# Kernel optimization log

Measured on AMD Instinct MI355X. Metric: run time of the kernel, lower is better.

The kernel has to match this reference:

```python
import jax, jax.numpy as jnp
import numpy as np

N, E, F_IN, F_OUT = 16384, 4096, 128, 128
EPS = 1e-6


def setup_inputs() -> dict:
    key = jax.random.key(0)
    k1, k2, k3 = jax.random.split(key, 3)
    H = (jax.random.uniform(k1, (N, E)) < 0.05).astype(jnp.float32)
    x = jax.random.normal(k2, (N, F_IN), dtype=jnp.float32)
    W = jax.random.normal(k3, (F_IN, F_OUT), dtype=jnp.float32) * 0.05
    return {"x": x, "H": H, "W": W}


def reference(x, H, W):
    # D_v^{-1} H D_e^{-1} H^T x W, computed without materializing the NxN
    # adjacency: diagonal matmuls become row/col broadcast scaling, and the
    # GEMM chain is reordered right-to-left (same math, associativity).
    d_e_inv = 1.0 / (H.sum(axis=0) + EPS)   # [E]
    d_v_inv = 1.0 / (H.sum(axis=1) + EPS)   # [N]
    xw = x @ W                               # [N, F_out]
    edge_msg = H.T @ xw                      # [E, F_out] gather onto edges
    edge_msg = d_e_inv[:, None] * edge_msg   # D_e^{-1}
    node_msg = H @ edge_msg                  # [N, F_out] scatter back to nodes
    return d_v_inv[:, None] * node_msg       # D_v^{-1}
```

## Files before the change

### kernel.cpp

```cpp
#include <hip/hip_runtime.h>
#include <stdint.h>

#define N_NODES 16384
#define N_EDGES 4096
#define FDIM    128
#define EPSF    1e-6f

typedef __attribute__((ext_vector_type(8))) short short8;
typedef __attribute__((ext_vector_type(4))) float f32x4;
typedef unsigned long long ull;

__device__ __forceinline__ unsigned short f2bf(float f) {
    uint32_t u = __float_as_uint(f);
    return (unsigned short)((u + 0x7FFFu + ((u >> 16) & 1u)) >> 16);
}
__device__ __forceinline__ short8 as_s8(uint4 v) {
    union { uint4 a; short8 b; } u; u.a = v; return u.b;
}

__device__ __forceinline__ short8 expand8(uint32_t half, int bitoff) {
    uint32_t b8 = (half >> bitoff) & 0xFFu;
    uint32_t lo = ((b8 & 0xFu) * 0x00204081u) & 0x01010101u;
    uint32_t hi = ((b8 >> 4) * 0x00204081u) & 0x01010101u;
    union { short8 v; uint32_t u[4]; } a;
#if __has_builtin(__builtin_amdgcn_perm)
    a.u[0] = __builtin_amdgcn_perm(0u, lo, 0x04010400u) * 0x3F80u;
    a.u[1] = __builtin_amdgcn_perm(0u, lo, 0x04030402u) * 0x3F80u;
    a.u[2] = __builtin_amdgcn_perm(0u, hi, 0x04010400u) * 0x3F80u;
    a.u[3] = __builtin_amdgcn_perm(0u, hi, 0x04030402u) * 0x3F80u;
#else
    a.u[0] = ((lo & 1u)         | ((lo >> 8) & 1u) << 16) * 0x3F80u;
    a.u[1] = (((lo >> 16) & 1u) | ((lo >> 24) & 1u) << 16) * 0x3F80u;
    a.u[2] = ((hi & 1u)         | ((hi >> 8) & 1u) << 16) * 0x3F80u;
    a.u[3] = (((hi >> 16) & 1u) | ((hi >> 24) & 1u) << 16) * 0x3F80u;
#endif
    return a.v;
}

__device__ __forceinline__ ull bit_transpose64(ull q, int lane) {
    const ull M32 = 0xFFFFFFFF00000000ull, M16 = 0xFFFF0000FFFF0000ull,
              M8 = 0xFF00FF00FF00FF00ull, M4 = 0xF0F0F0F0F0F0F0F0ull,
              M2 = 0xCCCCCCCCCCCCCCCCull, M1 = 0xAAAAAAAAAAAAAAAAull;
#define TSTEP(d, Md) { ull tv = __shfl_xor(q, d, 64); \
    q = ((lane & d) == 0) ? ((q & ~Md) | ((tv << d) & Md)) \
                          : ((q & Md) | ((tv >> d) & ~Md)); }
    TSTEP(32, M32) TSTEP(16, M16) TSTEP(8, M8) TSTEP(4, M4) TSTEP(2, M2) TSTEP(1, M1)
#undef TSTEP
    return q;
}

__global__ __launch_bounds__(256) void k_bitpack(const float* __restrict__ H,
        ull* __restrict__ bitsNE, float* __restrict__ dvinv) {
    int w = threadIdx.x >> 6, lane = threadIdx.x & 63;
    int n = blockIdx.x * 4 + w;
    const float4* hr = (const float4*)(H + (size_t)n * N_EDGES);
    ull* out = bitsNE + (size_t)n * (N_EDGES / 64);
    int cnt = 0;
    for (int c4 = 0; c4 < N_EDGES / 256; ++c4) {
        float4 v = hr[c4 * 64 + lane];
        ull b0 = __ballot(v.x > 0.5f);
        ull b1 = __ballot(v.y > 0.5f);
        ull b2 = __ballot(v.z > 0.5f);
        ull b3 = __ballot(v.w > 0.5f);
        cnt += __popcll(b0) + __popcll(b1) + __popcll(b2) + __popcll(b3);
        if (lane == 0) {
            #pragma unroll
            for (int q = 0; q < 4; ++q) {
                ull wq = ((b0 >> (16 * q)) & 0xFFFFull)
                       | (((b1 >> (16 * q)) & 0xFFFFull) << 16)
                       | (((b2 >> (16 * q)) & 0xFFFFull) << 32)
                       | (((b3 >> (16 * q)) & 0xFFFFull) << 48);
                out[c4 * 4 + q] = wq;
            }
        }
    }
    if (lane == 0) dvinv[n] = 1.0f / ((float)cnt + EPSF);
}

__global__ __launch_bounds__(256) void k_transpose_bf(const ull* __restrict__ bitsNE,
        ull* __restrict__ bitsEN) {
    int w = threadIdx.x >> 6, lane = threadIdx.x & 63;
    int wid = blockIdx.x * 4 + w;
    int nt = wid >> 3, etg = wid & 7;
    int pl = 4 * (lane & 15) + (lane >> 4);
    const ull* src = bitsNE + (size_t)(nt * 64 + pl) * (N_EDGES / 64);
    #pragma unroll
    for (int i = 0; i < 8; ++i) {
        int et = etg * 8 + i;
        ull q = src[et];
        q = bit_transpose64(q, lane);
        bitsEN[(size_t)(et * 64 + pl) * (N_NODES / 64) + nt] = q;
    }
}

__global__ __launch_bounds__(256) void k_edeg(const ull* __restrict__ bitsEN,
        float* __restrict__ deinv) {
    int w = threadIdx.x >> 6, lane = threadIdx.x & 63;
    int e = blockIdx.x * 4 + w;
    const ull* r = bitsEN + (size_t)e * (N_NODES / 64);
    int s = __popcll(r[lane]) + __popcll(r[lane + 64]) + __popcll(r[lane + 128]) + __popcll(r[lane + 192]);
    for (int o = 32; o; o >>= 1) s += __shfl_xor(s, o);
    if (lane == 0) deinv[e] = 1.0f / ((float)s + EPSF);
}

__global__ __launch_bounds__(256) void k_xw(const float* __restrict__ x, const float* __restrict__ W,
        unsigned short* __restrict__ xwTp) {
    __shared__ __attribute__((aligned(16))) unsigned short ldsWT[128 * 136];
    __shared__ __attribute__((aligned(16))) unsigned short ldsT[128 * 72];
    int t = threadIdx.x, lane = t & 63, w = t >> 6;
    int r16 = lane & 15, klane = lane >> 4;
    for (int i = 0; i < 64; ++i) {
        int idx = i * 256 + t;
        int k = idx >> 7, f = idx & 127;
        ldsWT[f * 136 + k] = f2bf(W[idx]);
    }
    __syncthreads();
    int nbase = blockIdx.x * 64;
    int row = nbase + w * 16 + r16;
    const float4* xr4 = (const float4*)(x + (size_t)row * FDIM);
    f32x4 acc[8] = {};
    for (int kb = 0; kb < 128; kb += 32) {
        float4 u0 = xr4[(kb >> 2) + klane * 2];
        float4 u1 = xr4[(kb >> 2) + klane * 2 + 1];
        union { short8 v; unsigned short u[8]; } a;
        a.u[0] = f2bf(u0.x); a.u[1] = f2bf(u0.y); a.u[2] = f2bf(u0.z); a.u[3] = f2bf(u0.w);
        a.u[4] = f2bf(u1.x); a.u[5] = f2bf(u1.y); a.u[6] = f2bf(u1.z); a.u[7] = f2bf(u1.w);
        #pragma unroll
        for (int fb = 0; fb < 8; ++fb) {
            short8 b = *(const short8*)&ldsWT[(fb * 16 + r16) * 136 + kb + klane * 8];
            acc[fb] = __builtin_amdgcn_mfma_f32_16x16x32_bf16(a.v, b, acc[fb], 0, 0, 0);
        }
    }
    #pragma unroll
    for (int fb = 0; fb < 8; ++fb)
        #pragma unroll
        for (int r = 0; r < 4; ++r)
            ldsT[(fb * 16 + r16) * 72 + 16 * r + w * 4 + klane] = f2bf(acc[fb][r]);
    __syncthreads();
    int f = t >> 1, part = t & 1;
    #pragma unroll
    for (int j = 0; j < 4; ++j)
        *(uint4*)&xwTp[(size_t)f * N_NODES + nbase + part * 32 + j * 8] =
            *(const uint4*)&ldsT[f * 72 + part * 32 + j * 8];
}

#define LOADP(Q0, Q1, BUF, p) do { \
    Q0 = brow0[(p)]; Q1 = brow1[(p)]; \
    const unsigned short* _src = bcol + (size_t)(p) * 64; \
    _Pragma("unroll") \
    for (int _fb = 0; _fb < 4; ++_fb) { \
        BUF[_fb * 2]     = *(const uint4*)(_src + _fb * fbstride); \
        BUF[_fb * 2 + 1] = *(const uint4*)(_src + _fb * fbstride + 32); \
    } } while (0)

#define COMPUTEP(Q0, Q1, BUF) do { \
    _Pragma("unroll") \
    for (int _s2 = 0; _s2 < 2; ++_s2) { \
        uint32_t _h0 = (uint32_t)(_s2 == 0 ? (Q0) : ((Q0) >> 32)); \
        uint32_t _h1 = (uint32_t)(_s2 == 0 ? (Q1) : ((Q1) >> 32)); \
        short8 _a0 = expand8(_h0, bitoff); \
        short8 _a1 = expand8(_h1, bitoff); \
        _Pragma("unroll") \
        for (int _f = 0; _f < 4; ++_f) { \
            short8 _b = as_s8(BUF[_f * 2 + _s2]); \
            acc[0][_f] = __builtin_amdgcn_mfma_f32_16x16x32_bf16(_a0, _b, acc[0][_f], 0, 0, 0); \
            acc[1][_f] = __builtin_amdgcn_mfma_f32_16x16x32_bf16(_a1, _b, acc[1][_f], 0, 0, 0); \
        } } } while (0)

template<bool FINAL, int NP>
__global__ __launch_bounds__(256) void k_gemm_gen(
        const ull* __restrict__ bits, int krows,
        const unsigned short* __restrict__ BT, int K,
        float* __restrict__ Cout, const float* __restrict__ rowScale, int M) {
    static_assert(NP % 3 == 1 || NP % 3 == 2, "tail requires NP%3 in {1,2}");
    int t = threadIdx.x, lane = t & 63, w = t >> 6;
    int r16 = lane & 15, klane = lane >> 4;
    int bitoff = klane * 8;
    int wm = w >> 1, wf = w & 1;
    int mbase = blockIdx.x * 64 + wm * 32;
    int kq0 = blockIdx.z * NP;
    const ull* brow0 = bits + (size_t)(mbase + r16) * krows + kq0;
    const ull* brow1 = brow0 + (size_t)16 * krows;
    const unsigned short* bcol = BT + (size_t)(wf * 64 + r16) * K + (size_t)kq0 * 64 + klane * 8;
    const size_t fbstride = (size_t)16 * K;
    f32x4 acc[2][4] = {};
    ull qA0, qA1, qB0, qB1, qC0, qC1;
    uint4 bufA[8], bufB[8], bufC[8];
    LOADP(qA0, qA1, bufA, 0);
    LOADP(qB0, qB1, bufB, 1);
    LOADP(qC0, qC1, bufC, 2);
    for (int p = 0; p <= NP - 7; p += 3) {
        COMPUTEP(qA0, qA1, bufA); LOADP(qA0, qA1, bufA, p + 3);
        COMPUTEP(qB0, qB1, bufB); LOADP(qB0, qB1, bufB, p + 4);
        COMPUTEP(qC0, qC1, bufC); LOADP(qC0, qC1, bufC, p + 5);
    }
    if constexpr (NP % 3 == 1) {
        COMPUTEP(qA0, qA1, bufA); LOADP(qA0, qA1, bufA, NP - 1);
        COMPUTEP(qB0, qB1, bufB);
        COMPUTEP(qC0, qC1, bufC);
        COMPUTEP(qA0, qA1, bufA);
    } else {
        COMPUTEP(qA0, qA1, bufA); LOADP(qA0, qA1, bufA, NP - 2);
        COMPUTEP(qB0, qB1, bufB); LOADP(qB0, qB1, bufB, NP - 1);
        COMPUTEP(qC0, qC1, bufC);
        COMPUTEP(qA0, qA1, bufA);
        COMPUTEP(qB0, qB1, bufB);
    }
    #pragma unroll
    for (int fr = 0; fr < 2; ++fr)
        #pragma unroll
        for (int fb = 0; fb < 4; ++fb)
            #pragma unroll
            for (int r = 0; r < 4; ++r) {
                int row = mbase + fr * 16 + klane * 4 + r;
                int col = wf * 64 + fb * 16 + r16;
                float v = acc[fr][fb][r];
                if (FINAL)
                    Cout[(size_t)row * FDIM + col] = rowScale[row] * v;
                else
                    Cout[(size_t)blockIdx.z * M * FDIM + (size_t)row * FDIM + col] = v;
            }
}

__global__ __launch_bounds__(256) void k_reduce_scale_T(const float* __restrict__ partials,
        const float* __restrict__ deinv, unsigned short* __restrict__ emTp, int S) {
    __shared__ float lds[64 * 129];
    int t = threadIdx.x;
    int e0 = blockIdx.x * 64;
    for (int i = 0; i < 32; ++i) {
        int idx = i * 256 + t;
        int e_l = idx >> 7, f = idx & 127;
        float s = 0.f;
        for (int z = 0; z < S; ++z)
            s += partials[(size_t)z * N_EDGES * FDIM + (size_t)(e0 + e_l) * FDIM + f];
        lds[e_l * 129 + f] = s * deinv[e0 + e_l];
    }
    __syncthreads();
    for (int i = 0; i < 32; ++i) {
        int idx = i * 256 + t;
        int f = idx >> 6, j = idx & 63;
        int pj = 4 * (j & 15) + (j >> 4);
        emTp[(size_t)f * N_EDGES + e0 + j] = f2bf(lds[pj * 129 + f]);
    }
}

__global__ __launch_bounds__(256) void k_finalN(const float* __restrict__ partN,
        const float* __restrict__ dvinv, float* __restrict__ out) {
    const float4* pa = (const float4*)partN;
    const float4* pb = (const float4*)(partN + (size_t)N_NODES * FDIM);
    float4* o4 = (float4*)out;
    int t = threadIdx.x;
    #pragma unroll
    for (int i = 0; i < 4; ++i) {
        int idx = blockIdx.x * 1024 + i * 256 + t;
        float4 a = pa[idx], b = pb[idx];
        float s = dvinv[idx >> 5];
        o4[idx] = make_float4((a.x + b.x) * s, (a.y + b.y) * s,
                              (a.z + b.z) * s, (a.w + b.w) * s);
    }
}

extern "C" void kernel_launch(void* const* d_in, const int* in_sizes, int n_in,
                              void* d_out, int out_size, void* d_ws, size_t ws_size,
                              hipStream_t stream) {
    const float* x = (const float*)d_in[0];
    const float* H = (const float*)d_in[1];
    const float* W = (const float*)d_in[2];
    float* out = (float*)d_out;
    char* ws = (char*)d_ws;

    ull* bitsNE = (ull*)(ws);
    ull* bitsEN = (ull*)(ws + (8u << 20));
    unsigned short* xwTp = (unsigned short*)(ws + (16u << 20));
    unsigned short* emTp = (unsigned short*)(ws + (20u << 20));
    float* dvinv = (float*)(ws + (21u << 20));
    float* deinv = (float*)(ws + (21u << 20) + 65536);
    float* partE = (float*)(ws + (22u << 20));
    float* partN = (float*)(ws + (38u << 20));

    bool big = ws_size >= ((38u << 20) + (size_t)2 * N_NODES * FDIM * 4);

    hipLaunchKernelGGL(k_bitpack, dim3(4096), dim3(256), 0, stream, H, bitsNE, dvinv);
    hipLaunchKernelGGL(k_transpose_bf, dim3(512), dim3(256), 0, stream, bitsNE, bitsEN);
    hipLaunchKernelGGL(k_edeg, dim3(1024), dim3(256), 0, stream, bitsEN, deinv);
    hipLaunchKernelGGL(k_xw, dim3(256), dim3(256), 0, stream, x, W, xwTp);
    if (big) {
        hipLaunchKernelGGL((k_gemm_gen<false, 32>), dim3(64, 1, 8), dim3(256), 0, stream,
                           bitsEN, N_NODES / 64, xwTp, N_NODES, partE, (const float*)nullptr,
                           N_EDGES);
        hipLaunchKernelGGL(k_reduce_scale_T, dim3(64), dim3(256), 0, stream, partE, deinv, emTp, 8);
        hipLaunchKernelGGL((k_gemm_gen<false, 32>), dim3(256, 1, 2), dim3(256), 0, stream,
                           bitsNE, N_EDGES / 64, emTp, N_EDGES, partN, (const float*)nullptr,
                           N_NODES);
        hipLaunchKernelGGL(k_finalN, dim3(512), dim3(256), 0, stream, partN, dvinv, out);
    } else {
        hipLaunchKernelGGL((k_gemm_gen<false, 64>), dim3(64, 1, 4), dim3(256), 0, stream,
                           bitsEN, N_NODES / 64, xwTp, N_NODES, partE, (const float*)nullptr,
                           N_EDGES);
        hipLaunchKernelGGL(k_reduce_scale_T, dim3(64), dim3(256), 0, stream, partE, deinv, emTp, 4);
        hipLaunchKernelGGL((k_gemm_gen<true, 64>), dim3(256, 1, 1), dim3(256), 0, stream,
                           bitsNE, N_EDGES / 64, emTp, N_EDGES, out, dvinv,
                           N_NODES);
    }
}
```

Baseline: 293.3 us.

## Use 512-thread edge GEMM and drop split-K partials for node GEMM

Adds a dedicated edge-side GEMM kernel using 512-thread blocks that cover 128 rows each, halving the block count along M. The node-side GEMM no longer uses a two-way split-K with a separate reduce kernel; it always runs the single-pass fused-scaling variant that writes the output directly. This removes one launch and the partial-sum round trip through memory, at the cost of less parallelism in the node GEMM and different occupancy in the edge GEMM.

```diff
diff --git a/kernel.cpp b/kernel.cpp
--- a/kernel.cpp
+++ b/kernel.cpp
@@ -222,6 +222,44 @@
             }
 }
 
+template<int NP>
+__global__ __launch_bounds__(512, 2) void k_gemm_edge(
+        const ull* __restrict__ bits, int krows,
+        const unsigned short* __restrict__ BT, int K,
+        float* __restrict__ Cout, int M) {
+    static_assert(NP % 2 == 0, "depth-2 loop requires even NP");
+    int t = threadIdx.x, lane = t & 63, w = t >> 6;
+    int r16 = lane & 15, klane = lane >> 4;
+    int bitoff = klane * 8;
+    int wm = w >> 1, wf = w & 1;
+    int mbase = blockIdx.x * 128 + wm * 32;
+    int kq0 = blockIdx.z * NP;
+    const ull* brow0 = bits + (size_t)(mbase + r16) * krows + kq0;
+    const ull* brow1 = brow0 + (size_t)16 * krows;
+    const unsigned short* bcol = BT + (size_t)(wf * 64 + r16) * K + (size_t)kq0 * 64 + klane * 8;
+    const size_t fbstride = (size_t)16 * K;
+    f32x4 acc[2][4] = {};
+    ull qA0, qA1, qB0, qB1;
+    uint4 bufA[8], bufB[8];
+    LOADP(qA0, qA1, bufA, 0);
+    for (int p = 0; p < NP; p += 2) {
+        LOADP(qB0, qB1, bufB, p + 1);
+        COMPUTEP(qA0, qA1, bufA);
+        if (p + 2 < NP) LOADP(qA0, qA1, bufA, p + 2);
+        COMPUTEP(qB0, qB1, bufB);
+    }
+    #pragma unroll
+    for (int fr = 0; fr < 2; ++fr)
+        #pragma unroll
+        for (int fb = 0; fb < 4; ++fb)
+            #pragma unroll
+            for (int r = 0; r < 4; ++r) {
+                int row = mbase + fr * 16 + klane * 4 + r;
+                int col = wf * 64 + fb * 16 + r16;
+                Cout[(size_t)blockIdx.z * M * FDIM + (size_t)row * FDIM + col] = acc[fr][fb][r];
+            }
+}
+
 __global__ __launch_bounds__(256) void k_reduce_scale_T(const float* __restrict__ partials,
         const float* __restrict__ deinv, unsigned short* __restrict__ emTp, int S) {
     __shared__ float lds[64 * 129];
@@ -244,22 +282,6 @@
     }
 }
 
-__global__ __launch_bounds__(256) void k_finalN(const float* __restrict__ partN,
-        const float* __restrict__ dvinv, float* __restrict__ out) {
-    const float4* pa = (const float4*)partN;
-    const float4* pb = (const float4*)(partN + (size_t)N_NODES * FDIM);
-    float4* o4 = (float4*)out;
-    int t = threadIdx.x;
-    #pragma unroll
-    for (int i = 0; i < 4; ++i) {
-        int idx = blockIdx.x * 1024 + i * 256 + t;
-        float4 a = pa[idx], b = pb[idx];
-        float s = dvinv[idx >> 5];
-        o4[idx] = make_float4((a.x + b.x) * s, (a.y + b.y) * s,
-                              (a.z + b.z) * s, (a.w + b.w) * s);
-    }
-}
-
 extern "C" void kernel_launch(void* const* d_in, const int* in_sizes, int n_in,
                               void* d_out, int out_size, void* d_ws, size_t ws_size,
                               hipStream_t stream) {
@@ -276,30 +298,24 @@
     float* dvinv = (float*)(ws + (21u << 20));
     float* deinv = (float*)(ws + (21u << 20) + 65536);
     float* partE = (float*)(ws + (22u << 20));
-    float* partN = (float*)(ws + (38u << 20));
-
-    bool big = ws_size >= ((38u << 20) + (size_t)2 * N_NODES * FDIM * 4);
+
+    bool big = ws_size >= ((22u << 20) + (size_t)8 * N_EDGES * FDIM * 4);
 
     hipLaunchKernelGGL(k_bitpack, dim3(4096), dim3(256), 0, stream, H, bitsNE, dvinv);
     hipLaunchKernelGGL(k_transpose_bf, dim3(512), dim3(256), 0, stream, bitsNE, bitsEN);
     hipLaunchKernelGGL(k_edeg, dim3(1024), dim3(256), 0, stream, bitsEN, deinv);
     hipLaunchKernelGGL(k_xw, dim3(256), dim3(256), 0, stream, x, W, xwTp);
     if (big) {
-        hipLaunchKernelGGL((k_gemm_gen<false, 32>), dim3(64, 1, 8), dim3(256), 0, stream,
-                           bitsEN, N_NODES / 64, xwTp, N_NODES, partE, (const float*)nullptr,
-                           N_EDGES);
+        hipLaunchKernelGGL((k_gemm_edge<32>), dim3(32, 1, 8), dim3(512), 0, stream,
+                           bitsEN, N_NODES / 64, xwTp, N_NODES, partE, N_EDGES);
         hipLaunchKernelGGL(k_reduce_scale_T, dim3(64), dim3(256), 0, stream, partE, deinv, emTp, 8);
-        hipLaunchKernelGGL((k_gemm_gen<false, 32>), dim3(256, 1, 2), dim3(256), 0, stream,
-                           bitsNE, N_EDGES / 64, emTp, N_EDGES, partN, (const float*)nullptr,
-                           N_NODES);
-        hipLaunchKernelGGL(k_finalN, dim3(512), dim3(256), 0, stream, partN, dvinv, out);
     } else {
         hipLaunchKernelGGL((k_gemm_gen<false, 64>), dim3(64, 1, 4), dim3(256), 0, stream,
                            bitsEN, N_NODES / 64, xwTp, N_NODES, partE, (const float*)nullptr,
                            N_EDGES);
         hipLaunchKernelGGL(k_reduce_scale_T, dim3(64), dim3(256), 0, stream, partE, deinv, emTp, 4);
-        hipLaunchKernelGGL((k_gemm_gen<true, 64>), dim3(256, 1, 1), dim3(256), 0, stream,
-                           bitsNE, N_EDGES / 64, emTp, N_EDGES, out, dvinv,
-                           N_NODES);
-    }
-}
+    }
+    hipLaunchKernelGGL((k_gemm_gen<true, 64>), dim3(256, 1, 1), dim3(256), 0, stream,
+                       bitsNE, N_EDGES / 64, emTp, N_EDGES, out, dvinv,
+                       N_NODES);
+}
```

Result: no change. 288.5 us (-1.7%).
